# Performance work log

Hardware: AMD Instinct MI355X
Metric: run time of the kernel (lower is better)

## Reference

```python
import jax, jax.numpy as jnp
import numpy as np

H_IMG, W_IMG = 128, 128            # image size (init arg)
FX, FY = 120.0, 120.0              # camera intrinsics (read from COLMAP cfg in original __init__)
CX, CY = 64.0, 64.0
N_GAUSS = 65536
N_POSES = 2
EPS = 1e-8


def quat2mat(q):
    q = q / jnp.linalg.norm(q)
    w, x, y, z = q[0], q[1], q[2], q[3]
    return jnp.stack([
        jnp.stack([1 - 2 * (y * y + z * z), 2 * (x * y - z * w), 2 * (x * z + y * w)]),
        jnp.stack([2 * (x * y + z * w), 1 - 2 * (x * x + z * z), 2 * (y * z - x * w)]),
        jnp.stack([2 * (x * z - y * w), 2 * (y * z + x * w), 1 - 2 * (x * x + y * y)]),
    ])


def _forward(positions, colors, opacities, scales, qvec, tvec, tile_hw, chunk_gauss):
    HW = H_IMG * W_IMG
    step = tile_hw * tile_hw          # pixels per tile (contiguous in flat row-major order)
    n_tiles = HW // step
    N = positions.shape[0]
    n_chunks = N // chunk_gauss
    xs = jnp.arange(W_IMG, dtype=jnp.float32)
    ys = jnp.arange(H_IMG, dtype=jnp.float32)
    yy, xx = jnp.meshgrid(ys, xs, indexing='ij')
    px = xx.reshape(-1)               # [HW] pixel x coords
    py = yy.reshape(-1)               # [HW] pixel y coords
    var_c = (scales[:, 0] ** 2).reshape(n_chunks, chunk_gauss)
    op_c = opacities[:, 0].reshape(n_chunks, chunk_gauss)
    col_c = colors.reshape(n_chunks, chunk_gauss, 3)

    def render_pose(q, t):
        R = quat2mat(q)
        cam = positions @ R.T + t                                 # [N,3] camera-space points
        uv = jnp.stack([cam[:, 0] / cam[:, 2] * FX + CX,
                        cam[:, 1] / cam[:, 2] * FY + CY], 1)      # [N,2] pixel-space centers
        uv_c = uv.reshape(n_chunks, chunk_gauss, 2)

        def body(acc, chunk):
            uvg, vg, og, cg = chunk                               # [C,2],[C],[C],[C,3]
            d2 = (px[None, :] - uvg[:, 0:1]) ** 2 + (py[None, :] - uvg[:, 1:2]) ** 2  # [C,HW]
            w = og[:, None] * jnp.exp(-0.5 * d2 / vg[:, None])    # [C,HW] splat weights
            return (acc[0] + w.T @ cg, acc[1] + w.sum(0)), None

        init = (jnp.zeros((HW, 3), jnp.float32), jnp.zeros((HW,), jnp.float32))
        (num, den), _ = jax.lax.scan(body, init, (uv_c, var_c, op_c, col_c))
        # original adds 1e-8 to the denominator once per gaussian chunk
        img = num / (den + n_chunks * EPS)[:, None]               # [HW,3] normalized blend
        # per tile of `step` flat pixels: [step,3].T -> [3,tile_hw,tile_hw]
        return img.reshape(n_tiles, step, 3).transpose(0, 2, 1).reshape(n_tiles, 3, tile_hw, tile_hw)

    out = jax.vmap(render_pose)(qvec, tvec)                       # [B, n_tiles, 3, th, th]
    return out.reshape(-1, 3, tile_hw, tile_hw)


def setup_inputs() -> dict:
    key = jax.random.key(0)
    ks = jax.random.split(key, 6)
    positions = jax.random.normal(ks[0], (N_GAUSS, 3), jnp.float32) * 1.5
    positions = positions.at[:, 2].set(jnp.abs(positions[:, 2]) + 4.0)  # keep z>0 (in front of camera)
    colors = jax.random.uniform(ks[1], (N_GAUSS, 3), jnp.float32)
    opacities = jax.random.uniform(ks[2], (N_GAUSS, 1), jnp.float32)
    scales = jax.random.uniform(ks[3], (N_GAUSS, 1), jnp.float32) * 2.0 + 1.0  # var strictly > 0
    qvec = jax.random.normal(ks[4], (N_POSES, 4), jnp.float32)
    tvec = jax.random.normal(ks[5], (N_POSES, 3), jnp.float32) * 0.1
    return {"positions": positions, "colors": colors, "opacities": opacities,
            "scales": scales, "qvec": qvec, "tvec": tvec,
            "tile_hw": 32, "chunk_gauss": 4096}


def reference(positions, colors, opacities, scales, qvec, tvec, tile_hw, chunk_gauss):
    return _forward(positions, colors, opacities, scales, qvec, tvec, tile_hw, chunk_gauss)
```

## Files before the change

kernel.cpp:

```cpp
#include <hip/hip_runtime.h>


#define H_IMG 128
#define W_IMG 128
#define FX_C 120.0f
#define FY_C 120.0f
#define CX_C 64.0f
#define CY_C 64.0f
#define NG 65536
#define SLAB 1024
#define KSPLIT 64
#define NCHUNK 16
#define APAD 72
#define NEG_HALF_LOG2E -0.72134752044448170f
#define EPS_TOT 1.6e-7f

#if __has_builtin(__builtin_amdgcn_exp2f)
#define EXP2(x) __builtin_amdgcn_exp2f(x)
#else
#define EXP2(x) exp2f(x)
#endif

typedef __attribute__((ext_vector_type(8))) short short8;
typedef __attribute__((ext_vector_type(4))) float f32x4;

__device__ __forceinline__ unsigned bfpk2(float a, float b) {
    return __builtin_amdgcn_perm(__float_as_uint(b) + 0x8000u,
                                 __float_as_uint(a) + 0x8000u,
                                 0x07060302u);
}

__global__ void zero_accum_kernel(float* __restrict__ p) {
    p[blockIdx.x * 256 + threadIdx.x] = 0.0f;
}

template <bool STORE>
__global__ __launch_bounds__(1024) void render_kernel(
    const float* __restrict__ gpos, const float* __restrict__ gcol,
    const float* __restrict__ gopa, const float* __restrict__ gscl,
    const float* __restrict__ qvec, const float* __restrict__ tvec,
    float* __restrict__ accum,
    float* __restrict__ pbuf)
{
    __shared__ ushort A_lds[64][APAD];
    __shared__ ushort B_lds[512][APAD];
    __shared__ float u_s[SLAB], v_s[SLAB], ke_s[SLAB];
    __shared__ float wc_s[4][SLAB];

    const int split = blockIdx.x;
    const int ph    = blockIdx.y;
    const int pose  = ph >> 1;
    const int half  = ph & 1;
    const int tid   = threadIdx.x;

    float q0 = qvec[pose*4+0], q1 = qvec[pose*4+1], q2 = qvec[pose*4+2], q3 = qvec[pose*4+3];
    float rn = rsqrtf(q0*q0 + q1*q1 + q2*q2 + q3*q3);
    float qw = q0*rn, qx = q1*rn, qy = q2*rn, qz = q3*rn;
    float r00 = 1.0f-2.0f*(qy*qy+qz*qz), r01 = 2.0f*(qx*qy-qz*qw), r02 = 2.0f*(qx*qz+qy*qw);
    float r10 = 2.0f*(qx*qy+qz*qw), r11 = 1.0f-2.0f*(qx*qx+qz*qz), r12 = 2.0f*(qy*qz-qx*qw);
    float r20 = 2.0f*(qx*qz-qy*qw), r21 = 2.0f*(qy*qz+qx*qw), r22 = 1.0f-2.0f*(qx*qx+qy*qy);
    float tx = tvec[pose*3+0], ty = tvec[pose*3+1], tz = tvec[pose*3+2];

    {
        int g = split*SLAB + tid;
        float p0 = gpos[g*3+0], p1 = gpos[g*3+1], p2 = gpos[g*3+2];
        float cxm = r00*p0 + r01*p1 + r02*p2 + tx;
        float cym = r10*p0 + r11*p1 + r12*p2 + ty;
        float czm = r20*p0 + r21*p1 + r22*p2 + tz;
        float iz  = 1.0f / czm;
        u_s[tid] = cxm*iz*FX_C + CX_C;
        v_s[tid] = cym*iz*FY_C + CY_C;
        float s  = gscl[g];
        ke_s[tid] = NEG_HALF_LOG2E / (s*s);
        float og = gopa[g];
        wc_s[0][tid] = og * gcol[g*3+0];
        wc_s[1][tid] = og * gcol[g*3+1];
        wc_s[2][tid] = og * gcol[g*3+2];
        wc_s[3][tid] = og;
    }
    __syncthreads();

    const int lane = tid & 63;
    const int wave = tid >> 6;
    const int kset = wave >> 3;
    const int wn8  = wave & 7;

    const bool isB = (tid < 512);
    const int st   = isB ? tid : (tid - 512);
    const int g4   = (st & 15) << 2;
    const int grp  = st >> 4;

    const int arow = lane & 15;
    const int kcol = kset*32 + ((lane >> 4) << 3);

    f32x4 acc[4][4] = {};

    for (int ch = 0; ch < NCHUNK; ++ch) {
        const int gb = (ch << 6) + g4;
        if (isB) {
            const float4 kv = *(const float4*)&ke_s[gb];
            const float4 uv = *(const float4*)&u_s[gb];
            float e[4][4];
            #pragma unroll
            for (int xi = 0; xi < 4; ++xi) {
                const float xf = (float)(grp*4 + xi);
                float d;
                d = xf - uv.x; e[xi][0] = EXP2(kv.x*d*d);
                d = xf - uv.y; e[xi][1] = EXP2(kv.y*d*d);
                d = xf - uv.z; e[xi][2] = EXP2(kv.z*d*d);
                d = xf - uv.w; e[xi][3] = EXP2(kv.w*d*d);
            }
            #pragma unroll
            for (int c = 0; c < 4; ++c) {
                const float4 wv = *(const float4*)&wc_s[c][gb];
                #pragma unroll
                for (int xi = 0; xi < 4; ++xi) {
                    uint2 pk;
                    pk.x = bfpk2(e[xi][0]*wv.x, e[xi][1]*wv.y);
                    pk.y = bfpk2(e[xi][2]*wv.z, e[xi][3]*wv.w);
                    *(uint2*)&B_lds[(c << 7) + grp*4 + xi][g4] = pk;
                }
            }
        } else {
            const float4 kv = *(const float4*)&ke_s[gb];
            const float4 vv = *(const float4*)&v_s[gb];
            #pragma unroll
            for (int yi = 0; yi < 2; ++yi) {
                const float yf = (float)(half*64 + grp*2 + yi);
                float d, f0, f1, f2, f3;
                d = yf - vv.x; f0 = EXP2(kv.x*d*d);
                d = yf - vv.y; f1 = EXP2(kv.y*d*d);
                d = yf - vv.z; f2 = EXP2(kv.z*d*d);
                d = yf - vv.w; f3 = EXP2(kv.w*d*d);
                uint2 pk;
                pk.x = bfpk2(f0, f1); pk.y = bfpk2(f2, f3);
                *(uint2*)&A_lds[grp*2 + yi][g4] = pk;
            }
        }
        __syncthreads();
        {
            short8 a[4], b[4];
            #pragma unroll
            for (int mt = 0; mt < 4; ++mt)
                a[mt] = *(const short8*)&A_lds[mt*16 + arow][kcol];
            #pragma unroll
            for (int nt = 0; nt < 4; ++nt)
                b[nt] = *(const short8*)&B_lds[wn8*64 + nt*16 + arow][kcol];
            #pragma unroll
            for (int mt = 0; mt < 4; ++mt)
                #pragma unroll
                for (int nt = 0; nt < 4; ++nt)
                    acc[mt][nt] = __builtin_amdgcn_mfma_f32_16x16x32_bf16(a[mt], b[nt], acc[mt][nt], 0, 0, 0);
        }
        __syncthreads();
    }

    f32x4* scr = (f32x4*)&B_lds[0][0];
    #pragma unroll
    for (int r = 0; r < 2; ++r) {
        if (kset == 1) {
            #pragma unroll
            for (int m2 = 0; m2 < 2; ++m2)
                #pragma unroll
                for (int nt = 0; nt < 4; ++nt)
                    scr[(((wn8*2 + m2)*4 + nt) << 6) + lane] = acc[r*2 + m2][nt];
        }
        __syncthreads();
        if (kset == 0) {
            #pragma unroll
            for (int m2 = 0; m2 < 2; ++m2)
                #pragma unroll
                for (int nt = 0; nt < 4; ++nt)
                    acc[r*2 + m2][nt] += scr[(((wn8*2 + m2)*4 + nt) << 6) + lane];
        }
        __syncthreads();
    }

    if (kset == 0) {
        const int m0 = (lane >> 4) << 2;
        const int n0 = wn8*64 + (lane & 15);
        if (STORE) {
            float* bp = pbuf + ((size_t)(ph*KSPLIT + split) * 64) * 512 + n0;
            #pragma unroll
            for (int mt = 0; mt < 4; ++mt)
                #pragma unroll
                for (int nt = 0; nt < 4; ++nt)
                    #pragma unroll
                    for (int r = 0; r < 4; ++r)
                        bp[(size_t)(mt*16 + m0 + r)*512 + nt*16] = acc[mt][nt][r];
        } else {
            float* bp = accum + ((size_t)(pose*H_IMG + half*64) * 512) + n0;
            #pragma unroll
            for (int mt = 0; mt < 4; ++mt)
                #pragma unroll
                for (int nt = 0; nt < 4; ++nt)
                    #pragma unroll
                    for (int r = 0; r < 4; ++r)
                        atomicAdd(bp + (size_t)(mt*16 + m0 + r)*512 + nt*16, acc[mt][nt][r]);
        }
    }
}

__global__ __launch_bounds__(1024) void reduce_norm_kernel(
    const float* __restrict__ pbuf, float* __restrict__ out)
{
    __shared__ float red[2][512];
    const int b  = blockIdx.x;
    const int p  = b >> 7;
    const int y  = b & 127;
    const int ph = p*2 + (y >> 6);
    const int yl = y & 63;
    const int t  = threadIdx.x;
    const int sg = t >> 9;
    const int n  = t & 511;

    const float* base = pbuf + ((size_t)(ph*KSPLIT + sg*32) * 64 + yl) * 512 + n;
    float s = 0.0f;
    #pragma unroll 8
    for (int i = 0; i < 32; ++i) s += base[(size_t)i * 32768];
    red[sg][n] = s;
    __syncthreads();

    if (t < 384) {
        const int c = t >> 7, x = t & 127;
        float den = red[0][384 + x] + red[1][384 + x];
        float num = red[0][t]       + red[1][t];
        float inv = 1.0f / (den + EPS_TOT);
        int tt = y >> 3;
        int q  = ((y & 7) << 7) + x;
        out[(size_t)((p*16 + tt)*3 + c) * 1024 + q] = num * inv;
    }
}

__global__ void normalize_kernel(const float* __restrict__ acc, float* __restrict__ out) {
    int idx = blockIdx.x * 256 + threadIdx.x;
    int x = idx & 127;
    int y = (idx >> 7) & 127;
    int p = idx >> 14;
    const float* base = acc + (size_t)(p*128 + y) * 512;
    float inv = 1.0f / (base[384 + x] + EPS_TOT);
    int t = y >> 3;
    int q = ((y & 7) << 7) + x;
    float* ob = out + (size_t)((p*16 + t)*3) * 1024 + q;
    ob[0]    = base[x]       * inv;
    ob[1024] = base[128 + x] * inv;
    ob[2048] = base[256 + x] * inv;
}

extern "C" void kernel_launch(void* const* d_in, const int* in_sizes, int n_in,
                              void* d_out, int out_size, void* d_ws, size_t ws_size,
                              hipStream_t stream) {
    const float* gpos = (const float*)d_in[0];
    const float* gcol = (const float*)d_in[1];
    const float* gopa = (const float*)d_in[2];
    const float* gscl = (const float*)d_in[3];
    const float* qv   = (const float*)d_in[4];
    const float* tv   = (const float*)d_in[5];
    float* out = (float*)d_out;

    const size_t need = (size_t)4 * KSPLIT * 64 * 512 * sizeof(float);

    if (ws_size >= need) {
        float* pbuf = (float*)d_ws;
        render_kernel<true><<<dim3(KSPLIT, 4), dim3(1024), 0, stream>>>(
            gpos, gcol, gopa, gscl, qv, tv, nullptr, pbuf);
        reduce_norm_kernel<<<dim3(256), dim3(1024), 0, stream>>>(pbuf, out);
    } else {
        float* acc = (float*)d_ws;
        zero_accum_kernel<<<dim3(512), dim3(256), 0, stream>>>(acc);
        render_kernel<false><<<dim3(KSPLIT, 4), dim3(1024), 0, stream>>>(
            gpos, gcol, gopa, gscl, qv, tv, acc, nullptr);
        normalize_kernel<<<dim3(128), dim3(256), 0, stream>>>(acc, out);
    }
}
```

Baseline: 114.9 us.

## Compute full image rows per block and store bf16 partial sums

Each block now covers all 128 image rows for one pose instead of half, with half as many gaussians per block and twice as many K-splits. This removes the duplicated x-factor (B matrix) exp work across the two halves and doubles A-tile reuse per B load. Partial sums are written to the workspace as bf16 instead of fp32 to cut write and reduce traffic, at the cost of summing 128 bf16-rounded partials. The accumulator array doubles, which raises register pressure.

Result: slower. 182.8 us (+59.1%).

```diff
diff --git a/kernel.cpp b/kernel.cpp
--- a/kernel.cpp
+++ b/kernel.cpp
@@ -8,9 +8,9 @@
 #define CX_C 64.0f
 #define CY_C 64.0f
 #define NG 65536
-#define SLAB 1024
-#define KSPLIT 64
-#define NCHUNK 16
+#define SLAB 512
+#define KSPLIT 128
+#define NCHUNK 8
 #define APAD 72
 #define NEG_HALF_LOG2E -0.72134752044448170f
 #define EPS_TOT 1.6e-7f
@@ -28,6 +28,9 @@
     return __builtin_amdgcn_perm(__float_as_uint(b) + 0x8000u,
                                  __float_as_uint(a) + 0x8000u,
                                  0x07060302u);
+}
+__device__ __forceinline__ ushort bf16u(float v) {
+    return (ushort)((__float_as_uint(v) + 0x8000u) >> 16);
 }
 
 __global__ void zero_accum_kernel(float* __restrict__ p) {
@@ -40,17 +43,15 @@
     const float* __restrict__ gopa, const float* __restrict__ gscl,
     const float* __restrict__ qvec, const float* __restrict__ tvec,
     float* __restrict__ accum,
-    float* __restrict__ pbuf)
+    ushort* __restrict__ pbuf)
 {
-    __shared__ ushort A_lds[64][APAD];
+    __shared__ ushort A_lds[H_IMG][APAD];
     __shared__ ushort B_lds[512][APAD];
     __shared__ float u_s[SLAB], v_s[SLAB], ke_s[SLAB];
     __shared__ float wc_s[4][SLAB];
 
     const int split = blockIdx.x;
-    const int ph    = blockIdx.y;
-    const int pose  = ph >> 1;
-    const int half  = ph & 1;
+    const int pose  = blockIdx.y;
     const int tid   = threadIdx.x;
 
     float q0 = qvec[pose*4+0], q1 = qvec[pose*4+1], q2 = qvec[pose*4+2], q3 = qvec[pose*4+3];
@@ -61,7 +62,7 @@
     float r20 = 2.0f*(qx*qz-qy*qw), r21 = 2.0f*(qy*qz+qx*qw), r22 = 1.0f-2.0f*(qx*qx+qy*qy);
     float tx = tvec[pose*3+0], ty = tvec[pose*3+1], tz = tvec[pose*3+2];
 
-    {
+    if (tid < SLAB) {
         int g = split*SLAB + tid;
         float p0 = gpos[g*3+0], p1 = gpos[g*3+1], p2 = gpos[g*3+2];
         float cxm = r00*p0 + r01*p1 + r02*p2 + tx;
@@ -86,19 +87,19 @@
     const int wn8  = wave & 7;
 
     const bool isB = (tid < 512);
-    const int st   = isB ? tid : (tid - 512);
+    const int st   = tid & 511;
     const int g4   = (st & 15) << 2;
     const int grp  = st >> 4;
 
-    const int arow = lane & 15;
+    const int frow = lane & 15;
     const int kcol = kset*32 + ((lane >> 4) << 3);
 
-    f32x4 acc[4][4] = {};
+    f32x4 acc[8][4] = {};
 
     for (int ch = 0; ch < NCHUNK; ++ch) {
         const int gb = (ch << 6) + g4;
+        const float4 kv = *(const float4*)&ke_s[gb];
         if (isB) {
-            const float4 kv = *(const float4*)&ke_s[gb];
             const float4 uv = *(const float4*)&u_s[gb];
             float e[4][4];
             #pragma unroll
@@ -122,11 +123,10 @@
                 }
             }
         } else {
-            const float4 kv = *(const float4*)&ke_s[gb];
             const float4 vv = *(const float4*)&v_s[gb];
             #pragma unroll
-            for (int yi = 0; yi < 2; ++yi) {
-                const float yf = (float)(half*64 + grp*2 + yi);
+            for (int yi = 0; yi < 4; ++yi) {
+                const float yf = (float)(grp*4 + yi);
                 float d, f0, f1, f2, f3;
                 d = yf - vv.x; f0 = EXP2(kv.x*d*d);
                 d = yf - vv.y; f1 = EXP2(kv.y*d*d);
@@ -134,20 +134,20 @@
                 d = yf - vv.w; f3 = EXP2(kv.w*d*d);
                 uint2 pk;
                 pk.x = bfpk2(f0, f1); pk.y = bfpk2(f2, f3);
-                *(uint2*)&A_lds[grp*2 + yi][g4] = pk;
+                *(uint2*)&A_lds[grp*4 + yi][g4] = pk;
             }
         }
         __syncthreads();
         {
-            short8 a[4], b[4];
-            #pragma unroll
-            for (int mt = 0; mt < 4; ++mt)
-                a[mt] = *(const short8*)&A_lds[mt*16 + arow][kcol];
+            short8 a[8], b[4];
+            #pragma unroll
+            for (int mt = 0; mt < 8; ++mt)
+                a[mt] = *(const short8*)&A_lds[mt*16 + frow][kcol];
             #pragma unroll
             for (int nt = 0; nt < 4; ++nt)
-                b[nt] = *(const short8*)&B_lds[wn8*64 + nt*16 + arow][kcol];
-            #pragma unroll
-            for (int mt = 0; mt < 4; ++mt)
+                b[nt] = *(const short8*)&B_lds[wn8*64 + nt*16 + frow][kcol];
+            #pragma unroll
+            for (int mt = 0; mt < 8; ++mt)
                 #pragma unroll
                 for (int nt = 0; nt < 4; ++nt)
                     acc[mt][nt] = __builtin_amdgcn_mfma_f32_16x16x32_bf16(a[mt], b[nt], acc[mt][nt], 0, 0, 0);
@@ -157,7 +157,7 @@
 
     f32x4* scr = (f32x4*)&B_lds[0][0];
     #pragma unroll
-    for (int r = 0; r < 2; ++r) {
+    for (int r = 0; r < 4; ++r) {
         if (kset == 1) {
             #pragma unroll
             for (int m2 = 0; m2 < 2; ++m2)
@@ -177,47 +177,48 @@
     }
 
     if (kset == 0) {
-        const int m0 = (lane >> 4) << 2;
+        const int q4 = (lane >> 4) << 2;
         const int n0 = wn8*64 + (lane & 15);
         if (STORE) {
-            float* bp = pbuf + ((size_t)(ph*KSPLIT + split) * 64) * 512 + n0;
-            #pragma unroll
-            for (int mt = 0; mt < 4; ++mt)
+            ushort* bp = pbuf + ((size_t)(pose*KSPLIT + split) * H_IMG) * 512 + n0;
+            #pragma unroll
+            for (int mt = 0; mt < 8; ++mt)
                 #pragma unroll
                 for (int nt = 0; nt < 4; ++nt)
                     #pragma unroll
                     for (int r = 0; r < 4; ++r)
-                        bp[(size_t)(mt*16 + m0 + r)*512 + nt*16] = acc[mt][nt][r];
+                        bp[(size_t)(mt*16 + q4 + r)*512 + nt*16] = bf16u(acc[mt][nt][r]);
         } else {
-            float* bp = accum + ((size_t)(pose*H_IMG + half*64) * 512) + n0;
-            #pragma unroll
-            for (int mt = 0; mt < 4; ++mt)
+            float* bp = accum + ((size_t)(pose*H_IMG) * 512) + n0;
+            #pragma unroll
+            for (int mt = 0; mt < 8; ++mt)
                 #pragma unroll
                 for (int nt = 0; nt < 4; ++nt)
                     #pragma unroll
                     for (int r = 0; r < 4; ++r)
-                        atomicAdd(bp + (size_t)(mt*16 + m0 + r)*512 + nt*16, acc[mt][nt][r]);
+                        atomicAdd(bp + (size_t)(mt*16 + q4 + r)*512 + nt*16, acc[mt][nt][r]);
         }
     }
 }
 
 __global__ __launch_bounds__(1024) void reduce_norm_kernel(
-    const float* __restrict__ pbuf, float* __restrict__ out)
+    const ushort* __restrict__ pbuf, float* __restrict__ out)
 {
     __shared__ float red[2][512];
     const int b  = blockIdx.x;
     const int p  = b >> 7;
     const int y  = b & 127;
-    const int ph = p*2 + (y >> 6);
-    const int yl = y & 63;
     const int t  = threadIdx.x;
     const int sg = t >> 9;
     const int n  = t & 511;
 
-    const float* base = pbuf + ((size_t)(ph*KSPLIT + sg*32) * 64 + yl) * 512 + n;
+    const ushort* base = pbuf + ((size_t)(p*KSPLIT + sg*64) * H_IMG + y) * 512 + n;
     float s = 0.0f;
     #pragma unroll 8
-    for (int i = 0; i < 32; ++i) s += base[(size_t)i * 32768];
+    for (int i = 0; i < 64; ++i) {
+        unsigned us = base[(size_t)i * (H_IMG*512)];
+        s += __uint_as_float(us << 16);
+    }
     red[sg][n] = s;
     __syncthreads();
 
@@ -258,17 +259,17 @@
     const float* tv   = (const float*)d_in[5];
     float* out = (float*)d_out;
 
-    const size_t need = (size_t)4 * KSPLIT * 64 * 512 * sizeof(float);
+    const size_t need = (size_t)2 * KSPLIT * H_IMG * 512 * sizeof(ushort);
 
     if (ws_size >= need) {
-        float* pbuf = (float*)d_ws;
-        render_kernel<true><<<dim3(KSPLIT, 4), dim3(1024), 0, stream>>>(
+        ushort* pbuf = (ushort*)d_ws;
+        render_kernel<true><<<dim3(KSPLIT, 2), dim3(1024), 0, stream>>>(
             gpos, gcol, gopa, gscl, qv, tv, nullptr, pbuf);
         reduce_norm_kernel<<<dim3(256), dim3(1024), 0, stream>>>(pbuf, out);
     } else {
         float* acc = (float*)d_ws;
         zero_accum_kernel<<<dim3(512), dim3(256), 0, stream>>>(acc);
-        render_kernel<false><<<dim3(KSPLIT, 4), dim3(1024), 0, stream>>>(
+        render_kernel<false><<<dim3(KSPLIT, 2), dim3(1024), 0, stream>>>(
             gpos, gcol, gopa, gscl, qv, tv, acc, nullptr);
         normalize_kernel<<<dim3(128), dim3(256), 0, stream>>>(acc, out);
     }
```
